# Kernel optimization log

Measured on AMD Instinct MI355X. Metric: run time of the kernel, lower is better.

## Reference

```python
import jax, jax.numpy as jnp
import numpy as np

T = 2048      # sequence length (single unbatched sequence)
V = 32000     # vocab
D = 1024      # d_model
E = 16        # number of experts (one structural group)
TOPK = 2      # router top-k
CAP = 256     # per-expert capacity (T*TOPK/E)
DFF = 2048    # expert MLP hidden
NHOPS = 2     # number of routing hops
EPS = 1e-5    # RMSNorm eps


def setup_inputs() -> dict:
    key = jax.random.key(0)
    ks = jax.random.split(key, 6)
    ids = jax.random.randint(ks[0], (T,), 0, V)
    embed_W = jax.random.normal(ks[1], (V, D), jnp.float32) * 0.02
    ln_scale = jnp.ones((D,), jnp.float32)
    router_W = jax.random.normal(ks[2], (NHOPS, D, E), jnp.float32) * (D ** -0.5)
    expert_W1 = jax.random.normal(ks[3], (NHOPS, E, D, DFF), jnp.float32) * (D ** -0.5)
    expert_W2 = jax.random.normal(ks[4], (NHOPS, E, DFF, D), jnp.float32) * (DFF ** -0.5)
    return dict(ids=ids, embed_W=embed_W, ln_scale=ln_scale,
                router_W=router_W, expert_W1=expert_W1, expert_W2=expert_W2)


def _hop(h, Wr, W1, W2):
    # Router: clean logits -> mixing probs (softmax) + hard top-k selection mask.
    logits = h @ Wr                                   # (T, E)
    probs = jax.nn.softmax(logits, axis=-1)           # (T, E)
    _, top = jax.lax.top_k(logits, TOPK)              # (T, TOPK)
    mask = jnp.zeros((T, E), bool).at[jnp.arange(T)[:, None], top].set(True)

    # _capacity_select: rank tokens per expert by clean logits, keep top CAP.
    m = mask.T                                        # (E, T)
    g = jnp.where(m, logits.T, -jnp.inf)              # (E, T)
    _, top_idx = jax.lax.top_k(g, CAP)                # (E, C)
    slot = jnp.zeros((E, CAP, T), h.dtype)
    slot = slot.at[jnp.arange(E)[:, None], jnp.arange(CAP)[None, :], top_idx].set(1.0)
    slot = slot * m[:, None, :].astype(h.dtype)       # zero slots filled from -inf
    kept = slot.sum(1) > 0                            # (E, T)

    # One-hot einsum gather of token states into expert slot buffers.
    xin = jnp.einsum('ect,td->ecd', slot, h)          # (E, C, D)

    # Stable sort slots by original token position (active slots first).
    active = slot.sum(-1) > 0                         # (E, C)
    pos = jnp.where(active, top_idx, T + 1)
    order = jnp.argsort(pos, axis=1, stable=True)     # (E, C)
    xin = jnp.take_along_axis(xin, order[:, :, None], axis=1)
    slot = jnp.take_along_axis(slot, order[:, :, None], axis=1)

    # Grouped (stacked/vmapped) expert execution: GELU MLP per expert.
    h1 = jax.nn.gelu(jnp.einsum('ecd,edf->ecf', xin, W1))
    expert_out = jnp.einsum('ecf,efd->ecd', h1, W2)   # (E, C, D)

    # Combine (Eq. 3): h_{s+1} = h_s + sum_e rho_e (M_e(h) - h)
    cw = jnp.where(kept.T, probs, 0.0)                # (T, E)
    rho = cw.sum(axis=1, keepdims=True)               # (T, 1)
    combine = jnp.einsum('ecd,ect,et->td', expert_out, slot, cw.T)
    return h + combine - rho * h


def reference(ids, embed_W, ln_scale, router_W, expert_W1, expert_W2):
    h = embed_W[ids]                                  # (T, D) embedding lookup
    for i in range(NHOPS):
        h = _hop(h, router_W[i], expert_W1[i], expert_W2[i])
    # RMSNorm + tied unembedding
    h = h * jax.lax.rsqrt(jnp.mean(h * h, axis=-1, keepdims=True) + EPS) * ln_scale
    return h @ embed_W.T                              # (T, V)
```

## Files before the change

### kernel.cpp

```cpp
#include <hip/hip_runtime.h>
#include <stdint.h>

#define T_ 2048
#define V_ 32000
#define D_ 1024
#define E_ 16
#define CAP_ 256
#define DFF_ 2048

typedef unsigned short u16;
typedef unsigned int u32;
typedef __bf16 bf16x8 __attribute__((ext_vector_type(8)));
typedef float f32x4 __attribute__((ext_vector_type(4)));

__device__ __forceinline__ u16 f2bf(float f){
  u32 u = __float_as_uint(f);
  u32 r = u + 0x7FFFu + ((u >> 16) & 1u);
  return (u16)(r >> 16);
}
__device__ __forceinline__ float bf2f(u16 s){ return __uint_as_float(((u32)s) << 16); }

__device__ __forceinline__ void gl_lds16(const void* g, void* l){
  __builtin_amdgcn_global_load_lds((const __attribute__((address_space(1))) void*)g,
                                   (__attribute__((address_space(3))) void*)l, 16, 0, 0);
}
__device__ __forceinline__ f32x4 mfma16(bf16x8 a, bf16x8 b, f32x4 c){
  return __builtin_amdgcn_mfma_f32_16x16x32_bf16(a, b, c, 0, 0, 0);
}
__device__ __forceinline__ float gelu_tanh(float x){
  float u = 0.7978845608028654f * (x + 0.044715f * x * x * x);
  return 0.5f * x * (1.0f + tanhf(u));
}

__global__ __launch_bounds__(256) void k_embed(const int* __restrict__ ids,
    const float* __restrict__ W, float* __restrict__ h){
  int t = blockIdx.x;
  int d = threadIdx.x * 4;
  *(float4*)(h + (size_t)t*D_ + d) = *(const float4*)(W + (size_t)ids[t]*D_ + d);
}

__global__ __launch_bounds__(256) void k_cvtw(const float* __restrict__ W, u16* __restrict__ Wb){
  size_t i = ((size_t)blockIdx.x*256 + threadIdx.x)*8;
  float4 a = *(const float4*)(W + i);
  float4 b = *(const float4*)(W + i + 4);
  union { u16 s[8]; uint4 v; } p;
  p.s[0]=f2bf(a.x); p.s[1]=f2bf(a.y); p.s[2]=f2bf(a.z); p.s[3]=f2bf(a.w);
  p.s[4]=f2bf(b.x); p.s[5]=f2bf(b.y); p.s[6]=f2bf(b.z); p.s[7]=f2bf(b.w);
  *(uint4*)(Wb + i) = p.v;
}

__global__ __launch_bounds__(256) void k_router(const float* __restrict__ h,
    const float* __restrict__ Wr, float* __restrict__ logits,
    unsigned char* __restrict__ mask, int* __restrict__ top2, float* __restrict__ p2){
  int w = threadIdx.x >> 6, l = threadIdx.x & 63;
  int t = blockIdx.x*4 + w;
  float acc[E_];
  #pragma unroll
  for (int e=0;e<E_;++e) acc[e]=0.f;
  const float* hrow = h + (size_t)t*D_;
  #pragma unroll
  for (int i=0;i<16;++i){
    int d = l + i*64;
    float hv = hrow[d];
    const float4* wr = (const float4*)(Wr + d*E_);
    float4 w0=wr[0], w1=wr[1], w2=wr[2], w3=wr[3];
    acc[0]+=hv*w0.x; acc[1]+=hv*w0.y; acc[2]+=hv*w0.z; acc[3]+=hv*w0.w;
    acc[4]+=hv*w1.x; acc[5]+=hv*w1.y; acc[6]+=hv*w1.z; acc[7]+=hv*w1.w;
    acc[8]+=hv*w2.x; acc[9]+=hv*w2.y; acc[10]+=hv*w2.z; acc[11]+=hv*w2.w;
    acc[12]+=hv*w3.x; acc[13]+=hv*w3.y; acc[14]+=hv*w3.z; acc[15]+=hv*w3.w;
  }
  #pragma unroll
  for (int off=32; off; off>>=1){
    #pragma unroll
    for (int e=0;e<E_;++e) acc[e] += __shfl_xor(acc[e], off, 64);
  }
  float mx = acc[0];
  #pragma unroll
  for (int e=1;e<E_;++e) mx = fmaxf(mx, acc[e]);
  float p[E_], s = 0.f;
  #pragma unroll
  for (int e=0;e<E_;++e){ p[e] = expf(acc[e]-mx); s += p[e]; }
  int i1 = 0; float v1 = acc[0];
  #pragma unroll
  for (int e=1;e<E_;++e) if (acc[e] > v1){ v1 = acc[e]; i1 = e; }
  int i2 = (i1==0)?1:0; float v2 = acc[i2];
  #pragma unroll
  for (int e=0;e<E_;++e) if (e!=i1 && e!=i2 && acc[e] > v2){ v2 = acc[e]; i2 = e; }
  if (l < E_){
    logits[t*E_+l] = acc[l];
    mask[t*E_+l] = (l==i1 || l==i2) ? 1 : 0;
  }
  if (l == 0){
    float inv = 1.f/s;
    top2[t*2] = i1; top2[t*2+1] = i2;
    p2[t*2] = p[i1]*inv; p2[t*2+1] = p[i2]*inv;
  }
}

__global__ __launch_bounds__(256) void k_init_etok(int* __restrict__ etok){
  etok[blockIdx.x*256 + threadIdx.x] = -1;
}

__global__ __launch_bounds__(256) void k_capacity(const float* __restrict__ logits,
    const unsigned char* __restrict__ mask, const int* __restrict__ top2,
    int* __restrict__ kept, int* __restrict__ etok){
  int w = threadIdx.x >> 6, l = threadIdx.x & 63;
  int wid = blockIdx.x*4 + w;
  int t = wid >> 1, k = wid & 1;
  int e = top2[t*2+k];
  float my = logits[t*E_+e];
  int cnt = 0;
  for (int t2 = l; t2 < T_; t2 += 64){
    if (mask[t2*E_+e]){
      float lg = logits[t2*E_+e];
      if (lg > my || (lg == my && t2 < t)) cnt++;
    }
  }
  #pragma unroll
  for (int off=32; off; off>>=1) cnt += __shfl_xor(cnt, off, 64);
  if (l == 0){
    if (cnt < CAP_){ kept[t*2+k] = cnt; etok[e*CAP_+cnt] = t; }
    else kept[t*2+k] = -1;
  }
}

__global__ __launch_bounds__(256) void k_gather(const float* __restrict__ h,
    const int* __restrict__ etok, u16* __restrict__ xhi, u16* __restrict__ xlo){
  int rc = blockIdx.x;
  int tok = etok[rc];
  int d = threadIdx.x * 4;
  float4 v = make_float4(0.f,0.f,0.f,0.f);
  if (tok >= 0) v = *(const float4*)(h + (size_t)tok*D_ + d);
  union { u16 s[4]; uint2 u; } hi, lo;
  hi.s[0]=f2bf(v.x); lo.s[0]=f2bf(v.x - bf2f(hi.s[0]));
  hi.s[1]=f2bf(v.y); lo.s[1]=f2bf(v.y - bf2f(hi.s[1]));
  hi.s[2]=f2bf(v.z); lo.s[2]=f2bf(v.z - bf2f(hi.s[2]));
  hi.s[3]=f2bf(v.w); lo.s[3]=f2bf(v.w - bf2f(hi.s[3]));
  *(uint2*)(xhi + (size_t)rc*D_ + d) = hi.u;
  *(uint2*)(xlo + (size_t)rc*D_ + d) = lo.u;
}

template<bool SPLIT, bool GELU>
__global__ __launch_bounds__(256, 2) void k_gemm_expert(
    const u16* __restrict__ Ahi, const u16* __restrict__ Alo,
    const float* __restrict__ Bw,
    u16* __restrict__ Ohi, u16* __restrict__ Olo, float* __restrict__ Of,
    int N, int K, int ntiles){
  constexpr int NB = SPLIT ? 2 : 1;
  __shared__ __align__(16) u16 As[NB*128*32];
  __shared__ __align__(16) u16 Bs[NB*128*40];
  u16* AsLo = As + 128*32;
  u16* BsLo = Bs + 128*40;
  int chunk = gridDim.x >> 3;
  int bid = blockIdx.x;
  int swz = (bid & 7)*chunk + (bid >> 3);
  int e = swz / (2*ntiles);
  int rem = swz - e*2*ntiles;
  int nt = rem >> 1, mt = rem & 1;
  int m0 = mt*128, n0 = nt*128;
  int tid = threadIdx.x;
  int l = tid & 63;
  int wr = tid >> 7, wc = (tid >> 6) & 1;
  int lr = l & 15, lq = l >> 4;
  int kb = tid >> 5, nb = tid & 31;
  const u16* Ah = Ahi + (size_t)e*256*K;
  const u16* Al = SPLIT ? (Alo + (size_t)e*256*K) : (const u16*)nullptr;
  const float* Bb = Bw + (size_t)e*K*N;
  f32x4 acc[4][4];
  #pragma unroll
  for (int i=0;i<4;++i)
    #pragma unroll
    for (int j=0;j<4;++j)
      #pragma unroll
      for (int c=0;c<4;++c) acc[i][j][c] = 0.f;

  float4 pb0, pb1, pb2, pb3;
  {
    const float* bs = Bb + (size_t)(kb*4)*N + n0 + nb*4;
    pb0 = *(const float4*)bs;
    pb1 = *(const float4*)(bs + N);
    pb2 = *(const float4*)(bs + 2*N);
    pb3 = *(const float4*)(bs + 3*N);
  }

  for (int k0 = 0; k0 < K; k0 += 32){
    __syncthreads();
    #pragma unroll
    for (int r=0;r<2;++r){
      int o = r*4096 + tid*16;
      int row = o >> 6;
      int c = (o >> 4) & 3;
      int cs = c ^ ((row >> 1) & 3);
      gl_lds16(Ah + (size_t)(m0+row)*K + k0 + cs*8, (char*)As + o);
      if constexpr (SPLIT)
        gl_lds16(Al + (size_t)(m0+row)*K + k0 + cs*8, (char*)AsLo + o);
    }
    {
      float cv[4][4] = {{pb0.x,pb1.x,pb2.x,pb3.x},{pb0.y,pb1.y,pb2.y,pb3.y},
                        {pb0.z,pb1.z,pb2.z,pb3.z},{pb0.w,pb1.w,pb2.w,pb3.w}};
      #pragma unroll
      for (int j=0;j<4;++j){
        int n = nb*4 + j;
        union { u16 s[4]; uint2 u; } hi, lo;
        #pragma unroll
        for (int i=0;i<4;++i){
          hi.s[i] = f2bf(cv[j][i]);
          if constexpr (SPLIT) lo.s[i] = f2bf(cv[j][i] - bf2f(hi.s[i]));
        }
        *(uint2*)((char*)Bs + n*80 + kb*8) = hi.u;
        if constexpr (SPLIT) *(uint2*)((char*)BsLo + n*80 + kb*8) = lo.u;
      }
    }
    if (k0 + 32 < K){
      const float* bs = Bb + (size_t)(k0 + 32 + kb*4)*N + n0 + nb*4;
      pb0 = *(const float4*)bs;
      pb1 = *(const float4*)(bs + N);
      pb2 = *(const float4*)(bs + 2*N);
      pb3 = *(const float4*)(bs + 3*N);
    }
    __syncthreads();
    bf16x8 ah[4], al[4], bh[4], bl[4];
    #pragma unroll
    for (int mi=0;mi<4;++mi){
      int row = wr*64 + mi*16 + lr;
      int q = lq ^ ((row >> 1) & 3);
      int o = row*64 + q*16;
      ah[mi] = *(const bf16x8*)((const char*)As + o);
      if constexpr (SPLIT) al[mi] = *(const bf16x8*)((const char*)AsLo + o);
    }
    #pragma unroll
    for (int ni=0;ni<4;++ni){
      int o = (wc*64 + ni*16 + lr)*80 + lq*16;
      bh[ni] = *(const bf16x8*)((const char*)Bs + o);
      if constexpr (SPLIT) bl[ni] = *(const bf16x8*)((const char*)BsLo + o);
    }
    #pragma unroll
    for (int mi=0;mi<4;++mi)
      #pragma unroll
      for (int ni=0;ni<4;++ni){
        acc[mi][ni] = mfma16(ah[mi], bh[ni], acc[mi][ni]);
        if constexpr (SPLIT){
          acc[mi][ni] = mfma16(al[mi], bh[ni], acc[mi][ni]);
          acc[mi][ni] = mfma16(ah[mi], bl[ni], acc[mi][ni]);
        }
      }
  }
  #pragma unroll
  for (int mi=0;mi<4;++mi)
    #pragma unroll
    for (int ni=0;ni<4;++ni)
      #pragma unroll
      for (int j=0;j<4;++j){
        int row = m0 + wr*64 + mi*16 + lq*4 + j;
        int col = n0 + wc*64 + ni*16 + lr;
        float x = acc[mi][ni][j];
        size_t idx = ((size_t)e*256 + row)*N + col;
        if constexpr (GELU){
          float y = gelu_tanh(x);
          u16 hv = f2bf(y);
          Ohi[idx] = hv;
          if constexpr (SPLIT) Olo[idx] = f2bf(y - bf2f(hv));
        } else {
          Of[idx] = x;
        }
      }
}

__global__ __launch_bounds__(256) void k_combine(float* __restrict__ h,
    const float* __restrict__ Y2, const int* __restrict__ top2,
    const float* __restrict__ p2, const int* __restrict__ kept){
  int t = blockIdx.x;
  int e0 = top2[t*2], e1 = top2[t*2+1];
  int r0 = kept[t*2], r1 = kept[t*2+1];
  float w0 = (r0 >= 0) ? p2[t*2]   : 0.f;
  float w1 = (r1 >= 0) ? p2[t*2+1] : 0.f;
  float om = 1.f - w0 - w1;
  int d = threadIdx.x * 4;
  float4 v = *(const float4*)(h + (size_t)t*D_ + d);
  float ox = v.x*om, oy = v.y*om, oz = v.z*om, ow = v.w*om;
  if (r0 >= 0){
    float4 y = *(const float4*)(Y2 + ((size_t)e0*CAP_ + r0)*D_ + d);
    ox += w0*y.x; oy += w0*y.y; oz += w0*y.z; ow += w0*y.w;
  }
  if (r1 >= 0){
    float4 y = *(const float4*)(Y2 + ((size_t)e1*CAP_ + r1)*D_ + d);
    ox += w1*y.x; oy += w1*y.y; oz += w1*y.z; ow += w1*y.w;
  }
  *(float4*)(h + (size_t)t*D_ + d) = make_float4(ox, oy, oz, ow);
}

__global__ __launch_bounds__(256) void k_rmsnorm(const float* __restrict__ h,
    const float* __restrict__ g, u16* __restrict__ hn){
  int t = blockIdx.x;
  int d = threadIdx.x * 4;
  int w = threadIdx.x >> 6, l = threadIdx.x & 63;
  __shared__ float red[4];
  float4 v = *(const float4*)(h + (size_t)t*D_ + d);
  float ss = v.x*v.x + v.y*v.y + v.z*v.z + v.w*v.w;
  #pragma unroll
  for (int off=32; off; off>>=1) ss += __shfl_xor(ss, off, 64);
  if (l == 0) red[w] = ss;
  __syncthreads();
  float tot = red[0] + red[1] + red[2] + red[3];
  float sc = rsqrtf(tot * (1.f/D_) + 1e-5f);
  float4 gs = *(const float4*)(g + d);
  union { u16 s[4]; uint2 u; } o;
  o.s[0] = f2bf(v.x*sc*gs.x); o.s[1] = f2bf(v.y*sc*gs.y);
  o.s[2] = f2bf(v.z*sc*gs.z); o.s[3] = f2bf(v.w*sc*gs.w);
  *(uint2*)(hn + (size_t)t*D_ + d) = o.u;
}

__global__ __launch_bounds__(256, 3) void k_gemm_final(const u16* __restrict__ A,
    const u16* __restrict__ B, float* __restrict__ C){
  __shared__ __align__(16) u16 As[128*64];
  __shared__ __align__(16) u16 Bs[128*64];
  int bid = blockIdx.x;
  int swz = (bid & 7)*500 + (bid >> 3);
  int m0 = (swz & 15) * 128;
  int n0 = (swz >> 4) * 128;
  int tid = threadIdx.x;
  int l = tid & 63;
  int wr = tid >> 7, wc = (tid >> 6) & 1;
  int lr = l & 15, lq = l >> 4;
  f32x4 acc[4][4];
  #pragma unroll
  for (int i=0;i<4;++i)
    #pragma unroll
    for (int j=0;j<4;++j)
      #pragma unroll
      for (int c=0;c<4;++c) acc[i][j][c] = 0.f;

  for (int k0 = 0; k0 < D_; k0 += 64){
    __syncthreads();
    #pragma unroll
    for (int r=0;r<4;++r){
      int o = r*4096 + tid*16;
      int row = o >> 7;
      int c = (o >> 4) & 7;
      int cs = c ^ (row & 7);
      gl_lds16(A + (size_t)(m0+row)*D_ + k0 + cs*8, (char*)As + o);
      gl_lds16(B + (size_t)(n0+row)*D_ + k0 + cs*8, (char*)Bs + o);
    }
    __syncthreads();
    #pragma unroll
    for (int kh=0; kh<2; ++kh){
      bf16x8 af[4], bf[4];
      #pragma unroll
      for (int mi=0;mi<4;++mi){
        int row = wr*64 + mi*16 + lr;
        int q = (lq + 4*kh) ^ (row & 7);
        af[mi] = *(const bf16x8*)((const char*)As + row*128 + q*16);
      }
      #pragma unroll
      for (int ni=0;ni<4;++ni){
        int row = wc*64 + ni*16 + lr;
        int q = (lq + 4*kh) ^ (row & 7);
        bf[ni] = *(const bf16x8*)((const char*)Bs + row*128 + q*16);
      }
      #pragma unroll
      for (int mi=0;mi<4;++mi)
        #pragma unroll
        for (int ni=0;ni<4;++ni)
          acc[mi][ni] = mfma16(af[mi], bf[ni], acc[mi][ni]);
    }
  }
  #pragma unroll
  for (int mi=0;mi<4;++mi)
    #pragma unroll
    for (int ni=0;ni<4;++ni)
      #pragma unroll
      for (int j=0;j<4;++j){
        int row = m0 + wr*64 + mi*16 + lq*4 + j;
        int col = n0 + wc*64 + ni*16 + lr;
        C[(size_t)row * V_ + col] = acc[mi][ni][j];
      }
}

extern "C" void kernel_launch(void* const* d_in, const int* in_sizes, int n_in,
                              void* d_out, int out_size, void* d_ws, size_t ws_size,
                              hipStream_t stream){
  const int*   ids  = (const int*)d_in[0];
  const float* embW = (const float*)d_in[1];
  const float* lns  = (const float*)d_in[2];
  const float* WrA  = (const float*)d_in[3];
  const float* W1A  = (const float*)d_in[4];
  const float* W2A  = (const float*)d_in[5];
  float* out = (float*)d_out;
  char* ws = (char*)d_ws;
  const size_t MB = 1u << 20;

  float* h      = (float*)(ws);
  float* logits = (float*)(ws + 8*MB);
  unsigned char* mask = (unsigned char*)(ws + 8*MB + 131072);
  int*   top2v  = (int*)(ws + 8*MB + 131072 + 32768);
  float* p2     = (float*)(ws + 8*MB + 131072 + 32768 + 16384);
  int*   kept   = (int*)(ws + 8*MB + 131072 + 32768 + 32768);
  int*   etok   = (int*)(ws + 8*MB + 131072 + 32768 + 49152);
  u16*   xhi  = (u16*)(ws + 9*MB);
  u16*   xlo  = (u16*)(ws + 17*MB);
  float* y2   = (float*)(ws + 9*MB);
  u16*   y1hi = (u16*)(ws + 25*MB);
  u16*   y1lo = (u16*)(ws + 41*MB);
  u16*   hn   = (u16*)(ws + 57*MB);
  u16*   ebf  = (u16*)(ws + 61*MB);

  k_embed<<<T_, 256, 0, stream>>>(ids, embW, h);
  k_cvtw<<<(V_*D_)/(256*8), 256, 0, stream>>>(embW, ebf);

  for (int hop = 0; hop < 2; ++hop){
    const float* Wr = WrA + (size_t)hop*D_*E_;
    const float* W1 = W1A + (size_t)hop*E_*D_*DFF_;
    const float* W2 = W2A + (size_t)hop*E_*DFF_*D_;
    k_router<<<T_/4, 256, 0, stream>>>(h, Wr, logits, mask, top2v, p2);
    k_init_etok<<<E_*CAP_/256, 256, 0, stream>>>(etok);
    k_capacity<<<T_*2/4, 256, 0, stream>>>(logits, mask, top2v, kept, etok);
    k_gather<<<E_*CAP_, 256, 0, stream>>>(h, etok, xhi, xlo);
    if (hop == 0){
      k_gemm_expert<true , true ><<<E_*2*(DFF_/128), 256, 0, stream>>>(
          xhi, xlo, W1, y1hi, y1lo, nullptr, DFF_, D_, DFF_/128);
      k_gemm_expert<true , false><<<E_*2*(D_/128), 256, 0, stream>>>(
          y1hi, y1lo, W2, nullptr, nullptr, y2, D_, DFF_, D_/128);
    } else {
      k_gemm_expert<false, true ><<<E_*2*(DFF_/128), 256, 0, stream>>>(
          xhi, nullptr, W1, y1hi, nullptr, nullptr, DFF_, D_, DFF_/128);
      k_gemm_expert<false, false><<<E_*2*(D_/128), 256, 0, stream>>>(
          y1hi, nullptr, W2, nullptr, nullptr, y2, D_, DFF_, D_/128);
    }
    k_combine<<<T_, 256, 0, stream>>>(h, y2, top2v, p2, kept);
  }

  k_rmsnorm<<<T_, 256, 0, stream>>>(h, lns, hn);
  k_gemm_final<<<(T_/128)*(V_/128), 256, 0, stream>>>(hn, ebf, out);
}
```

Before: 665.9 us.

## Rewrite final unembedding GEMM with 256x256 tiles and 4-stage LDS pipeline

The final T×V unembedding GEMM now uses 256×256 output tiles with 512 threads. It streams K in 32-wide slices through a 4-slot LDS ring using direct global-to-LDS loads, with explicit vmcnt waits and a single barrier per step, so loads overlap MFMA compute. The larger tiles raise arithmetic intensity and cut redundant global reads of A and B. In exchange each block uses 128KB of LDS and more accumulator registers, which may limit occupancy, and the workgroup remap assumes exact divisibility of the grid.

```diff
diff --git a/kernel.cpp b/kernel.cpp
--- a/kernel.cpp
+++ b/kernel.cpp
@@ -310,68 +310,98 @@
   *(uint2*)(hn + (size_t)t*D_ + d) = o.u;
 }
 
-__global__ __launch_bounds__(256, 3) void k_gemm_final(const u16* __restrict__ A,
+#define SLOT_ 16384
+__global__ __launch_bounds__(512, 2) void k_gemm_final(const u16* __restrict__ A,
     const u16* __restrict__ B, float* __restrict__ C){
-  __shared__ __align__(16) u16 As[128*64];
-  __shared__ __align__(16) u16 Bs[128*64];
+  __shared__ __align__(16) char lds[131072];
+  char* ldsA = lds;
+  char* ldsB = lds + 65536;
   int bid = blockIdx.x;
-  int swz = (bid & 7)*500 + (bid >> 3);
-  int m0 = (swz & 15) * 128;
-  int n0 = (swz >> 4) * 128;
+  int wgid = (bid & 7) * 125 + (bid >> 3);
+  int m0 = (wgid & 7) << 8;
+  int n0 = (wgid >> 3) << 8;
   int tid = threadIdx.x;
-  int l = tid & 63;
-  int wr = tid >> 7, wc = (tid >> 6) & 1;
-  int lr = l & 15, lq = l >> 4;
-  f32x4 acc[4][4];
-  #pragma unroll
-  for (int i=0;i<4;++i)
+  int lane = tid & 63;
+  int w = tid >> 6;
+  int wm = w >> 2, wn = w & 3;
+  int lr = lane & 15, lq = lane >> 4;
+
+  f32x4 acc[8][4];
+  #pragma unroll
+  for (int i=0;i<8;++i)
     #pragma unroll
     for (int j=0;j<4;++j)
       #pragma unroll
       for (int c=0;c<4;++c) acc[i][j][c] = 0.f;
 
-  for (int k0 = 0; k0 < D_; k0 += 64){
-    __syncthreads();
-    #pragma unroll
-    for (int r=0;r<4;++r){
-      int o = r*4096 + tid*16;
-      int row = o >> 7;
-      int c = (o >> 4) & 7;
-      int cs = c ^ (row & 7);
-      gl_lds16(A + (size_t)(m0+row)*D_ + k0 + cs*8, (char*)As + o);
-      gl_lds16(B + (size_t)(n0+row)*D_ + k0 + cs*8, (char*)Bs + o);
-    }
-    __syncthreads();
-    #pragma unroll
-    for (int kh=0; kh<2; ++kh){
-      bf16x8 af[4], bf[4];
-      #pragma unroll
-      for (int mi=0;mi<4;++mi){
-        int row = wr*64 + mi*16 + lr;
-        int q = (lq + 4*kh) ^ (row & 7);
-        af[mi] = *(const bf16x8*)((const char*)As + row*128 + q*16);
-      }
-      #pragma unroll
-      for (int ni=0;ni<4;++ni){
-        int row = wc*64 + ni*16 + lr;
-        int q = (lq + 4*kh) ^ (row & 7);
-        bf[ni] = *(const bf16x8*)((const char*)Bs + row*128 + q*16);
-      }
-      #pragma unroll
-      for (int mi=0;mi<4;++mi)
-        #pragma unroll
-        for (int ni=0;ni<4;++ni)
-          acc[mi][ni] = mfma16(af[mi], bf[ni], acc[mi][ni]);
-    }
-  }
-  #pragma unroll
-  for (int mi=0;mi<4;++mi)
+  int j_0 = w*2, j_1 = w*2 + 1;
+  int rp0 = j_0*8 + (lane>>3), rp1 = j_1*8 + (lane>>3);
+  int c80 = (lane&7) ^ (rp0&7), c81 = (lane&7) ^ (rp1&7);
+  int rA0 = rp0*2 + (c80>>2), rA1 = rp1*2 + (c81>>2);
+  int cc0 = (c80&3)*8,        cc1 = (c81&3)*8;
+  const u16* sA0 = A + (size_t)(m0+rA0)*D_ + cc0;
+  const u16* sA1 = A + (size_t)(m0+rA1)*D_ + cc1;
+  const u16* sB0 = B + (size_t)(n0+rA0)*D_ + cc0;
+  const u16* sB1 = B + (size_t)(n0+rA1)*D_ + cc1;
+  int d0 = j_0*1024 + lane*16, d1 = j_1*1024 + lane*16;
+
+  int aoff[8], boff[4];
+  #pragma unroll
+  for (int mi=0;mi<8;++mi){
+    int r = wm*128 + mi*16 + lr;
+    int rp = r >> 1;
+    int c8 = ((r&1)<<2) | lq;
+    aoff[mi] = rp*128 + ((c8 ^ (rp&7))<<4);
+  }
+  #pragma unroll
+  for (int ni=0;ni<4;++ni){
+    int r = wn*64 + ni*16 + lr;
+    int rp = r >> 1;
+    int c8 = ((r&1)<<2) | lq;
+    boff[ni] = rp*128 + ((c8 ^ (rp&7))<<4);
+  }
+
+  #define STAGE_(sbase) do { \
+    gl_lds16(sA0, ldsA + (sbase) + d0); gl_lds16(sB0, ldsB + (sbase) + d0); \
+    gl_lds16(sA1, ldsA + (sbase) + d1); gl_lds16(sB1, ldsB + (sbase) + d1); \
+    sA0 += 32; sA1 += 32; sB0 += 32; sB1 += 32; } while(0)
+
+  STAGE_(0); STAGE_(SLOT_); STAGE_(2*SLOT_);
+
+  for (int kh = 0; kh < 32; ++kh){
+    if (kh < 30)       asm volatile("s_waitcnt vmcnt(8)" ::: "memory");
+    else if (kh == 30) asm volatile("s_waitcnt vmcnt(4)" ::: "memory");
+    else               asm volatile("s_waitcnt vmcnt(0)" ::: "memory");
+    __builtin_amdgcn_sched_barrier(0);
+    __builtin_amdgcn_s_barrier();
+    __builtin_amdgcn_sched_barrier(0);
+    if (kh <= 28) STAGE_(((kh+3)&3)*SLOT_);
+    int sb = (kh & 3) * SLOT_;
+    const char* pA = ldsA + sb;
+    const char* pB = ldsB + sb;
+    bf16x8 b[4];
+    #pragma unroll
+    for (int ni=0;ni<4;++ni) b[ni] = *(const bf16x8*)(pB + boff[ni]);
+    __builtin_amdgcn_s_setprio(1);
+    #pragma unroll
+    for (int mi=0;mi<8;++mi){
+      bf16x8 a = *(const bf16x8*)(pA + aoff[mi]);
+      #pragma unroll
+      for (int ni=0;ni<4;++ni)
+        acc[mi][ni] = mfma16(a, b[ni], acc[mi][ni]);
+    }
+    __builtin_amdgcn_s_setprio(0);
+  }
+  #undef STAGE_
+
+  #pragma unroll
+  for (int mi=0;mi<8;++mi)
     #pragma unroll
     for (int ni=0;ni<4;++ni)
       #pragma unroll
       for (int j=0;j<4;++j){
-        int row = m0 + wr*64 + mi*16 + lq*4 + j;
-        int col = n0 + wc*64 + ni*16 + lr;
+        int row = m0 + wm*128 + mi*16 + lq*4 + j;
+        int col = n0 + wn*64 + ni*16 + lr;
         C[(size_t)row * V_ + col] = acc[mi][ni][j];
       }
 }
@@ -430,5 +460,5 @@
   }
 
   k_rmsnorm<<<T_, 256, 0, stream>>>(h, lns, hn);
-  k_gemm_final<<<(T_/128)*(V_/128), 256, 0, stream>>>(hn, ebf, out);
-}
+  k_gemm_final<<<(T_/256)*(V_/256), 512, 0, stream>>>(hn, ebf, out);
+}
```

After: 676.9 us. About the same (+1.6%).
